# Optimization experiments

Measured on AMD Instinct MI355X. Metric: run time of the kernel, lower is better.

## Reference

```python
import jax, jax.numpy as jnp
import numpy as np

FP4_E2M1_VALUES = jnp.array([0.0, 0.5, 1.0, 1.5, 2.0, 3.0, 4.0, 6.0,
                             -0.0, -0.5, -1.0, -1.5, -2.0, -3.0, -4.0, -6.0],
                            dtype=jnp.float32)

OUT_F, IN_F, BS = 4096, 4096, 16


def setup_inputs() -> dict:
    key = jax.random.key(0)
    k1, k2, k3, k4 = jax.random.split(key, 4)
    x = jax.random.normal(k1, (4, 2048, IN_F), dtype=jnp.float32)
    weight_indices = jax.random.randint(k2, (OUT_F, IN_F // BS, BS), 0, 16, dtype=jnp.int32)
    weight_scales = jax.random.uniform(k3, (OUT_F, IN_F // BS), dtype=jnp.float32)
    bias = jax.random.normal(k4, (OUT_F,), dtype=jnp.float32)
    return {"x": x, "weight_indices": weight_indices,
            "weight_scales": weight_scales, "bias": bias}


def reference(x, weight_indices, weight_scales, bias):
    # Dequantize: gather FP4 values per index, scale per block of 16.
    idx = jnp.clip(weight_indices, 0, 15)              # [O, NB, BS]
    vals = FP4_E2M1_VALUES[idx]                        # [O, NB, BS]
    weight = (vals * weight_scales[:, :, None]).reshape(OUT_F, IN_F)
    # F.linear: y = x @ W^T + b
    return jnp.einsum('bsi,oi->bso', x, weight) + bias
```

## Files before the change

### kernel.cpp

```cpp
#include <hip/hip_runtime.h>
#include <hip/hip_bf16.h>

static constexpr int M_TOT = 8192;
static constexpr int N_TOT = 4096;
static constexpr int K_TOT = 4096;

static constexpr int BM = 256, BN = 256, BK = 32;
static constexpr int NT = K_TOT / BK;
static constexpr int GTHREADS = 512;
static constexpr int BUF_BYTES = 32768;
static constexpr int LDS_BYTES = 4 * BUF_BYTES;

typedef __bf16 bf16x8 __attribute__((ext_vector_type(8)));
typedef float f32x4 __attribute__((ext_vector_type(4)));
typedef unsigned short u16x8 __attribute__((ext_vector_type(8)));

__device__ __forceinline__ unsigned short f2bf(float f) {
  return __builtin_bit_cast(unsigned short, (__bf16)f);
}

__device__ __forceinline__ float fp4_decode(int idx) {
  unsigned u = (unsigned)idx & 15u;
  unsigned sgn = (u >> 3) << 31;
  unsigned mag = u & 7u;
  unsigned e = mag >> 1, m = mag & 1u;
  unsigned bits = (e == 0u) ? (m ? 0x3F000000u : 0u)
                            : (((126u + e) << 23) | (m << 22));
  return __uint_as_float(bits | sgn);
}

__device__ __forceinline__ void glds16(const void* g, void* l) {
  __builtin_amdgcn_global_load_lds(
      (__attribute__((address_space(1))) void*)g,
      (__attribute__((address_space(3))) void*)l, 16, 0, 0);
}

__global__ __launch_bounds__(256) void dequant_w_kernel(
    const int* __restrict__ idx, const float* __restrict__ scales,
    unsigned short* __restrict__ W) {
  const int t = blockIdx.x * 256 + threadIdx.x;
  const int4 v = reinterpret_cast<const int4*>(idx)[t];
  const float s = scales[t >> 2];
  ushort4 o;
  o.x = f2bf(fp4_decode(v.x) * s);
  o.y = f2bf(fp4_decode(v.y) * s);
  o.z = f2bf(fp4_decode(v.z) * s);
  o.w = f2bf(fp4_decode(v.w) * s);
  reinterpret_cast<ushort4*>(W)[t] = o;
}

__global__ __launch_bounds__(256) void convert_x_kernel(
    const float* __restrict__ x, unsigned short* __restrict__ A) {
  const int t = blockIdx.x * 256 + threadIdx.x;
  const float4* xp = reinterpret_cast<const float4*>(x);
  const float4 a = xp[2 * t], b = xp[2 * t + 1];
  u16x8 o;
  o[0] = f2bf(a.x); o[1] = f2bf(a.y); o[2] = f2bf(a.z); o[3] = f2bf(a.w);
  o[4] = f2bf(b.x); o[5] = f2bf(b.y); o[6] = f2bf(b.z); o[7] = f2bf(b.w);
  reinterpret_cast<u16x8*>(A)[t] = o;
}

__global__ __launch_bounds__(GTHREADS, 1) void gemm256(
    const unsigned short* __restrict__ A, const unsigned short* __restrict__ B,
    const float* __restrict__ bias, float* __restrict__ out) {
  extern __shared__ char smem[];

  const int t = threadIdx.x;
  const int lane = t & 63, wid = t >> 6;
  const int wr = wid >> 2;
  const int wc = wid & 3;
  const int ln = lane & 15;
  const int kc = lane >> 4;

  const int bid = blockIdx.x;
  const int bmi = (bid & 7) * 4 + ((bid >> 3) & 3);
  const int bni = bid >> 5;
  const int bm0 = bmi * BM, bn0 = bni * BN;

  const int row_s = t >> 2;
  const int kcd = (t & 3) ^ ((t >> 3) & 3);
  const unsigned short* gA = A + (size_t)(bm0 + row_s) * K_TOT + kcd * 8;
  const unsigned short* gB = B + (size_t)(bn0 + row_s) * K_TOT + kcd * 8;
  char* ldsA = smem + t * 16;
  char* ldsB = smem + 16384 + t * 16;

  const int swz = (kc ^ ((ln >> 1) & 3)) * 16;
  const int base_a = (wr * 128 + ln) * 64 + swz;
  const int base_b = 16384 + (wc * 64 + ln) * 64 + swz;

  f32x4 acc[8][4];
#pragma unroll
  for (int i = 0; i < 8; ++i)
#pragma unroll
    for (int j = 0; j < 4; ++j) acc[i][j] = f32x4{0.f, 0.f, 0.f, 0.f};

#define STAGE_A(kt, bufi) do {                                        \
    const unsigned short* s_ = gA + (size_t)(kt) * BK;                \
    glds16(s_, ldsA + (bufi) * BUF_BYTES);                            \
    glds16(s_ + (size_t)128 * K_TOT, ldsA + (bufi) * BUF_BYTES + 8192); \
  } while (0)
#define STAGE_B(kt, bufi) do {                                        \
    const unsigned short* s_ = gB + (size_t)(kt) * BK;                \
    glds16(s_, ldsB + (bufi) * BUF_BYTES);                            \
    glds16(s_ + (size_t)128 * K_TOT, ldsB + (bufi) * BUF_BYTES + 8192); \
  } while (0)

  bf16x8 af[4], bf[4];

#define LOAD_A4(bufi, mb) do {                                        \
    const char* pa_ = smem + (bufi) * BUF_BYTES + base_a + (mb) * 1024; \
    af[0] = *(const bf16x8*)(pa_);                                    \
    af[1] = *(const bf16x8*)(pa_ + 1024);                             \
    af[2] = *(const bf16x8*)(pa_ + 2048);                             \
    af[3] = *(const bf16x8*)(pa_ + 3072);                             \
  } while (0)
#define LOAD_B4(bufi) do {                                            \
    const char* pb_ = smem + (bufi) * BUF_BYTES + base_b;             \
    bf[0] = *(const bf16x8*)(pb_);                                    \
    bf[1] = *(const bf16x8*)(pb_ + 1024);                             \
    bf[2] = *(const bf16x8*)(pb_ + 2048);                             \
    bf[3] = *(const bf16x8*)(pb_ + 3072);                             \
  } while (0)

#define MFMA16(mb) do {                                               \
    __builtin_amdgcn_s_setprio(1);                                    \
    _Pragma("unroll")                                                 \
    for (int m_ = 0; m_ < 4; ++m_)                                    \
      _Pragma("unroll")                                               \
      for (int n_ = 0; n_ < 4; ++n_)                                  \
        acc[(mb) + m_][n_] = __builtin_amdgcn_mfma_f32_16x16x32_bf16( \
            af[m_], bf[n_], acc[(mb) + m_][n_], 0, 0, 0);             \
    __builtin_amdgcn_s_setprio(0);                                    \
  } while (0)

  STAGE_A(0, 0); STAGE_B(0, 0);
  asm volatile("" ::: "memory");
  STAGE_A(1, 1); STAGE_B(1, 1);
  asm volatile("" ::: "memory");
  STAGE_A(2, 2); STAGE_B(2, 2);
  asm volatile("s_waitcnt vmcnt(8)" ::: "memory");
  __builtin_amdgcn_s_barrier();

  for (int tt = 0; tt < NT - 3; ++tt) {
    const int cb = tt & 3, sb = (tt + 3) & 3;
    LOAD_A4(cb, 0);
    LOAD_B4(cb);
    STAGE_A(tt + 3, sb);
    __builtin_amdgcn_s_barrier();
    MFMA16(0);
    __builtin_amdgcn_s_barrier();
    LOAD_A4(cb, 4);
    STAGE_B(tt + 3, sb);
    __builtin_amdgcn_s_barrier();
    MFMA16(4);
    asm volatile("s_waitcnt vmcnt(8)" ::: "memory");
    __builtin_amdgcn_s_barrier();
  }

  for (int tt = NT - 3; tt < NT; ++tt) {
    const int cb = tt & 3;
    LOAD_A4(cb, 0);
    LOAD_B4(cb);
    __builtin_amdgcn_s_barrier();
    MFMA16(0);
    __builtin_amdgcn_s_barrier();
    LOAD_A4(cb, 4);
    __builtin_amdgcn_s_barrier();
    MFMA16(4);
    if (tt == NT - 3) asm volatile("s_waitcnt vmcnt(4)" ::: "memory");
    else if (tt == NT - 2) asm volatile("s_waitcnt vmcnt(0)" ::: "memory");
    __builtin_amdgcn_s_barrier();
  }

  const int orow0 = bm0 + wr * 128 + (lane >> 4) * 4;
  const int ocol0 = bn0 + wc * 64 + ln;
  float bj[4];
#pragma unroll
  for (int n = 0; n < 4; ++n) bj[n] = bias[ocol0 + n * 16];
#pragma unroll
  for (int mi = 0; mi < 8; ++mi)
#pragma unroll
    for (int n = 0; n < 4; ++n)
#pragma unroll
      for (int q = 0; q < 4; ++q)
        out[(size_t)(orow0 + mi * 16 + q) * N_TOT + ocol0 + n * 16] =
            acc[mi][n][q] + bj[n];
}

extern "C" void kernel_launch(void* const* d_in, const int* in_sizes, int n_in,
                              void* d_out, int out_size, void* d_ws, size_t ws_size,
                              hipStream_t stream) {
  const float* x = (const float*)d_in[0];
  const int* widx = (const int*)d_in[1];
  const float* wsc = (const float*)d_in[2];
  const float* bias = (const float*)d_in[3];
  float* out = (float*)d_out;

  unsigned short* Abf = (unsigned short*)d_ws;
  unsigned short* Wbf = (unsigned short*)((char*)d_ws + (size_t)M_TOT * K_TOT * 2);

  convert_x_kernel<<<dim3((M_TOT * (size_t)K_TOT / 8) / 256), dim3(256), 0, stream>>>(x, Abf);
  dequant_w_kernel<<<dim3((N_TOT * (size_t)K_TOT / 4) / 256), dim3(256), 0, stream>>>(widx, wsc, Wbf);

  (void)hipFuncSetAttribute((const void*)gemm256,
                            hipFuncAttributeMaxDynamicSharedMemorySize, LDS_BYTES);
  gemm256<<<dim3((M_TOT / BM) * (N_TOT / BN)), dim3(GTHREADS), LDS_BYTES, stream>>>(
      Abf, Wbf, bias, out);
}
```

Measured before the change: 292.7 us.

## Software-pipeline LDS fragment reads with double-buffered registers in GEMM main loop

```diff
diff --git a/kernel.cpp b/kernel.cpp
--- a/kernel.cpp
+++ b/kernel.cpp
@@ -94,43 +94,60 @@
 #pragma unroll
     for (int j = 0; j < 4; ++j) acc[i][j] = f32x4{0.f, 0.f, 0.f, 0.f};
 
-#define STAGE_A(kt, bufi) do {                                        \
-    const unsigned short* s_ = gA + (size_t)(kt) * BK;                \
-    glds16(s_, ldsA + (bufi) * BUF_BYTES);                            \
+  bf16x8 afA[4], afB[4], bfE[4], bfO[4];
+
+#define STAGE_A(kt, bufi) do {                                          \
+    const unsigned short* s_ = gA + (size_t)(kt) * BK;                  \
+    glds16(s_, ldsA + (bufi) * BUF_BYTES);                              \
     glds16(s_ + (size_t)128 * K_TOT, ldsA + (bufi) * BUF_BYTES + 8192); \
   } while (0)
-#define STAGE_B(kt, bufi) do {                                        \
-    const unsigned short* s_ = gB + (size_t)(kt) * BK;                \
-    glds16(s_, ldsB + (bufi) * BUF_BYTES);                            \
+#define STAGE_B(kt, bufi) do {                                          \
+    const unsigned short* s_ = gB + (size_t)(kt) * BK;                  \
+    glds16(s_, ldsB + (bufi) * BUF_BYTES);                              \
     glds16(s_ + (size_t)128 * K_TOT, ldsB + (bufi) * BUF_BYTES + 8192); \
   } while (0)
 
-  bf16x8 af[4], bf[4];
-
-#define LOAD_A4(bufi, mb) do {                                        \
-    const char* pa_ = smem + (bufi) * BUF_BYTES + base_a + (mb) * 1024; \
-    af[0] = *(const bf16x8*)(pa_);                                    \
-    af[1] = *(const bf16x8*)(pa_ + 1024);                             \
-    af[2] = *(const bf16x8*)(pa_ + 2048);                             \
-    af[3] = *(const bf16x8*)(pa_ + 3072);                             \
-  } while (0)
-#define LOAD_B4(bufi) do {                                            \
-    const char* pb_ = smem + (bufi) * BUF_BYTES + base_b;             \
-    bf[0] = *(const bf16x8*)(pb_);                                    \
-    bf[1] = *(const bf16x8*)(pb_ + 1024);                             \
-    bf[2] = *(const bf16x8*)(pb_ + 2048);                             \
-    bf[3] = *(const bf16x8*)(pb_ + 3072);                             \
-  } while (0)
-
-#define MFMA16(mb) do {                                               \
-    __builtin_amdgcn_s_setprio(1);                                    \
-    _Pragma("unroll")                                                 \
-    for (int m_ = 0; m_ < 4; ++m_)                                    \
-      _Pragma("unroll")                                               \
-      for (int n_ = 0; n_ < 4; ++n_)                                  \
-        acc[(mb) + m_][n_] = __builtin_amdgcn_mfma_f32_16x16x32_bf16( \
-            af[m_], bf[n_], acc[(mb) + m_][n_], 0, 0, 0);             \
-    __builtin_amdgcn_s_setprio(0);                                    \
+#define READ_AF(dst, bufi, mb) do {                                     \
+    const char* p_ = smem + (bufi) * BUF_BYTES + base_a + (mb) * 1024;  \
+    dst[0] = *(const bf16x8*)(p_);                                      \
+    dst[1] = *(const bf16x8*)(p_ + 1024);                               \
+    dst[2] = *(const bf16x8*)(p_ + 2048);                               \
+    dst[3] = *(const bf16x8*)(p_ + 3072);                               \
+  } while (0)
+#define READ_BF(dst, bufi) do {                                         \
+    const char* p_ = smem + (bufi) * BUF_BYTES + base_b;                \
+    dst[0] = *(const bf16x8*)(p_);                                      \
+    dst[1] = *(const bf16x8*)(p_ + 1024);                               \
+    dst[2] = *(const bf16x8*)(p_ + 2048);                               \
+    dst[3] = *(const bf16x8*)(p_ + 3072);                               \
+  } while (0)
+
+#define MFMA16(afs, bfs, mb) do {                                       \
+    __builtin_amdgcn_s_setprio(1);                                      \
+    _Pragma("unroll")                                                   \
+    for (int m_ = 0; m_ < 4; ++m_)                                      \
+      _Pragma("unroll")                                                 \
+      for (int n_ = 0; n_ < 4; ++n_)                                    \
+        acc[(mb) + m_][n_] = __builtin_amdgcn_mfma_f32_16x16x32_bf16(   \
+            afs[m_], bfs[n_], acc[(mb) + m_][n_], 0, 0, 0);             \
+    __builtin_amdgcn_s_setprio(0);                                      \
+  } while (0)
+
+#define VM(n) asm volatile("s_waitcnt vmcnt(" #n ")" ::: "memory")
+#define BAR __builtin_amdgcn_s_barrier()
+
+#define PH_A(tt, rb, sb, bfc) do { \
+    READ_AF(afB, rb, 4);           \
+    STAGE_A((tt) + 3, sb);         \
+    MFMA16(afA, bfc, 0);           \
+    VM(6); BAR;                    \
+  } while (0)
+#define PH_B(tt, rbn, sb, bfc, bfn) do { \
+    READ_AF(afA, rbn, 0);                \
+    READ_BF(bfn, rbn);                   \
+    STAGE_B((tt) + 3, sb);               \
+    MFMA16(afB, bfc, 4);                 \
+    BAR;                                 \
   } while (0)
 
   STAGE_A(0, 0); STAGE_B(0, 0);
@@ -138,39 +155,31 @@
   STAGE_A(1, 1); STAGE_B(1, 1);
   asm volatile("" ::: "memory");
   STAGE_A(2, 2); STAGE_B(2, 2);
-  asm volatile("s_waitcnt vmcnt(8)" ::: "memory");
-  __builtin_amdgcn_s_barrier();
-
-  for (int tt = 0; tt < NT - 3; ++tt) {
-    const int cb = tt & 3, sb = (tt + 3) & 3;
-    LOAD_A4(cb, 0);
-    LOAD_B4(cb);
-    STAGE_A(tt + 3, sb);
-    __builtin_amdgcn_s_barrier();
-    MFMA16(0);
-    __builtin_amdgcn_s_barrier();
-    LOAD_A4(cb, 4);
-    STAGE_B(tt + 3, sb);
-    __builtin_amdgcn_s_barrier();
-    MFMA16(4);
-    asm volatile("s_waitcnt vmcnt(8)" ::: "memory");
-    __builtin_amdgcn_s_barrier();
+  VM(8);
+  BAR;
+  READ_AF(afA, 0, 0);
+  READ_BF(bfE, 0);
+
+#pragma unroll 1
+  for (int tt = 0; tt < NT - 4; tt += 4) {
+    PH_A(tt + 0, 0, 3, bfE);
+    PH_B(tt + 0, 1, 3, bfE, bfO);
+    PH_A(tt + 1, 1, 0, bfO);
+    PH_B(tt + 1, 2, 0, bfO, bfE);
+    PH_A(tt + 2, 2, 1, bfE);
+    PH_B(tt + 2, 3, 1, bfE, bfO);
+    PH_A(tt + 3, 3, 2, bfO);
+    PH_B(tt + 3, 0, 2, bfO, bfE);
   }
 
-  for (int tt = NT - 3; tt < NT; ++tt) {
-    const int cb = tt & 3;
-    LOAD_A4(cb, 0);
-    LOAD_B4(cb);
-    __builtin_amdgcn_s_barrier();
-    MFMA16(0);
-    __builtin_amdgcn_s_barrier();
-    LOAD_A4(cb, 4);
-    __builtin_amdgcn_s_barrier();
-    MFMA16(4);
-    if (tt == NT - 3) asm volatile("s_waitcnt vmcnt(4)" ::: "memory");
-    else if (tt == NT - 2) asm volatile("s_waitcnt vmcnt(0)" ::: "memory");
-    __builtin_amdgcn_s_barrier();
-  }
+  READ_AF(afB, 0, 4); STAGE_A(127, 3); MFMA16(afA, bfE, 0); VM(6); BAR;
+  READ_AF(afA, 1, 0); READ_BF(bfO, 1); STAGE_B(127, 3); MFMA16(afB, bfE, 4); BAR;
+  READ_AF(afB, 1, 4); MFMA16(afA, bfO, 0); VM(4); BAR;
+  READ_AF(afA, 2, 0); READ_BF(bfE, 2); MFMA16(afB, bfO, 4); BAR;
+  READ_AF(afB, 2, 4); MFMA16(afA, bfE, 0); VM(0); BAR;
+  READ_AF(afA, 3, 0); READ_BF(bfO, 3); MFMA16(afB, bfE, 4); BAR;
+  READ_AF(afB, 3, 4); MFMA16(afA, bfO, 0);
+  MFMA16(afB, bfO, 4);
 
   const int orow0 = bm0 + wr * 128 + (lane >> 4) * 4;
   const int ocol0 = bn0 + wc * 64 + ln;
```

Measured after the change: 279.2 us. 4.6% less time.

## Shrink GEMM tile to 128x256 with 3-stage pipeline and higher occupancy

Applied to the files above, without the earlier changes.

```diff
diff --git a/kernel.cpp b/kernel.cpp
--- a/kernel.cpp
+++ b/kernel.cpp
@@ -5,11 +5,11 @@
 static constexpr int N_TOT = 4096;
 static constexpr int K_TOT = 4096;
 
-static constexpr int BM = 256, BN = 256, BK = 32;
+static constexpr int BM = 128, BN = 256, BK = 32;
 static constexpr int NT = K_TOT / BK;
 static constexpr int GTHREADS = 512;
-static constexpr int BUF_BYTES = 32768;
-static constexpr int LDS_BYTES = 4 * BUF_BYTES;
+static constexpr int BUF_BYTES = 24576;
+static constexpr int LDS_BYTES = 3 * BUF_BYTES;
 
 typedef __bf16 bf16x8 __attribute__((ext_vector_type(8)));
 typedef float f32x4 __attribute__((ext_vector_type(4)));
@@ -60,125 +60,110 @@
   reinterpret_cast<u16x8*>(A)[t] = o;
 }
 
-__global__ __launch_bounds__(GTHREADS, 1) void gemm256(
+__global__ __launch_bounds__(GTHREADS, 4) void gemm128x256(
     const unsigned short* __restrict__ A, const unsigned short* __restrict__ B,
     const float* __restrict__ bias, float* __restrict__ out) {
   extern __shared__ char smem[];
 
   const int t = threadIdx.x;
   const int lane = t & 63, wid = t >> 6;
-  const int wr = wid >> 2;
-  const int wc = wid & 3;
-  const int ln = lane & 15;
+  const int wrm = wid >> 2;
+  const int wcn = wid & 3;
+  const int l15 = lane & 15;
   const int kc = lane >> 4;
 
   const int bid = blockIdx.x;
-  const int bmi = (bid & 7) * 4 + ((bid >> 3) & 3);
-  const int bni = bid >> 5;
+  const int bmi = (bid & 7) * 8 + ((bid >> 3) & 7);
+  const int bni = bid >> 6;
   const int bm0 = bmi * BM, bn0 = bni * BN;
 
   const int row_s = t >> 2;
   const int kcd = (t & 3) ^ ((t >> 3) & 3);
   const unsigned short* gA = A + (size_t)(bm0 + row_s) * K_TOT + kcd * 8;
   const unsigned short* gB = B + (size_t)(bn0 + row_s) * K_TOT + kcd * 8;
-  char* ldsA = smem + t * 16;
-  char* ldsB = smem + 16384 + t * 16;
+  const unsigned short* gB1 = gB + (size_t)128 * K_TOT;
+  const int tid16 = t * 16;
 
-  const int swz = (kc ^ ((ln >> 1) & 3)) * 16;
-  const int base_a = (wr * 128 + ln) * 64 + swz;
-  const int base_b = 16384 + (wc * 64 + ln) * 64 + swz;
+  const int swz = (kc ^ ((l15 >> 1) & 3)) * 16;
+  const int base_a = (wrm * 64 + l15) * 64 + swz;
+  const int base_b = 8192 + (wcn * 64 + l15) * 64 + swz;
 
-  f32x4 acc[8][4];
+  f32x4 acc[4][4];
 #pragma unroll
-  for (int i = 0; i < 8; ++i)
+  for (int i = 0; i < 4; ++i)
 #pragma unroll
     for (int j = 0; j < 4; ++j) acc[i][j] = f32x4{0.f, 0.f, 0.f, 0.f};
 
-#define STAGE_A(kt, bufi) do {                                        \
-    const unsigned short* s_ = gA + (size_t)(kt) * BK;                \
-    glds16(s_, ldsA + (bufi) * BUF_BYTES);                            \
-    glds16(s_ + (size_t)128 * K_TOT, ldsA + (bufi) * BUF_BYTES + 8192); \
-  } while (0)
-#define STAGE_B(kt, bufi) do {                                        \
-    const unsigned short* s_ = gB + (size_t)(kt) * BK;                \
-    glds16(s_, ldsB + (bufi) * BUF_BYTES);                            \
-    glds16(s_ + (size_t)128 * K_TOT, ldsB + (bufi) * BUF_BYTES + 8192); \
+  bf16x8 af[4], bf[4];
+
+#define STG(kt, soff) do {                                   \
+    const int ko_ = (kt) * BK;                               \
+    glds16(gA + ko_, smem + (soff) + tid16);                 \
+    glds16(gB + ko_, smem + (soff) + 8192 + tid16);          \
+    glds16(gB1 + ko_, smem + (soff) + 16384 + tid16);        \
   } while (0)
 
-  bf16x8 af[4], bf[4];
-
-#define LOAD_A4(bufi, mb) do {                                        \
-    const char* pa_ = smem + (bufi) * BUF_BYTES + base_a + (mb) * 1024; \
-    af[0] = *(const bf16x8*)(pa_);                                    \
-    af[1] = *(const bf16x8*)(pa_ + 1024);                             \
-    af[2] = *(const bf16x8*)(pa_ + 2048);                             \
-    af[3] = *(const bf16x8*)(pa_ + 3072);                             \
-  } while (0)
-#define LOAD_B4(bufi) do {                                            \
-    const char* pb_ = smem + (bufi) * BUF_BYTES + base_b;             \
-    bf[0] = *(const bf16x8*)(pb_);                                    \
-    bf[1] = *(const bf16x8*)(pb_ + 1024);                             \
-    bf[2] = *(const bf16x8*)(pb_ + 2048);                             \
-    bf[3] = *(const bf16x8*)(pb_ + 3072);                             \
+#define RD(cboff) do {                                       \
+    const char* pa_ = smem + (cboff) + base_a;               \
+    const char* pb_ = smem + (cboff) + base_b;               \
+    af[0] = *(const bf16x8*)(pa_);                           \
+    af[1] = *(const bf16x8*)(pa_ + 1024);                    \
+    af[2] = *(const bf16x8*)(pa_ + 2048);                    \
+    af[3] = *(const bf16x8*)(pa_ + 3072);                    \
+    bf[0] = *(const bf16x8*)(pb_);                           \
+    bf[1] = *(const bf16x8*)(pb_ + 1024);                    \
+    bf[2] = *(const bf16x8*)(pb_ + 2048);                    \
+    bf[3] = *(const bf16x8*)(pb_ + 3072);                    \
   } while (0)
 
-#define MFMA16(mb) do {                                               \
-    __builtin_amdgcn_s_setprio(1);                                    \
-    _Pragma("unroll")                                                 \
-    for (int m_ = 0; m_ < 4; ++m_)                                    \
-      _Pragma("unroll")                                               \
-      for (int n_ = 0; n_ < 4; ++n_)                                  \
-        acc[(mb) + m_][n_] = __builtin_amdgcn_mfma_f32_16x16x32_bf16( \
-            af[m_], bf[n_], acc[(mb) + m_][n_], 0, 0, 0);             \
-    __builtin_amdgcn_s_setprio(0);                                    \
+#define MF16() do {                                          \
+    __builtin_amdgcn_s_setprio(1);                           \
+    _Pragma("unroll")                                        \
+    for (int m_ = 0; m_ < 4; ++m_)                           \
+      _Pragma("unroll")                                      \
+      for (int n_ = 0; n_ < 4; ++n_)                         \
+        acc[m_][n_] = __builtin_amdgcn_mfma_f32_16x16x32_bf16( \
+            af[m_], bf[n_], acc[m_][n_], 0, 0, 0);           \
+    __builtin_amdgcn_s_setprio(0);                           \
   } while (0)
 
-  STAGE_A(0, 0); STAGE_B(0, 0);
+#define VM(n) asm volatile("s_waitcnt vmcnt(" #n ")" ::: "memory")
+#define BAR __builtin_amdgcn_s_barrier()
+
+#define PH(tt, cboff, sboff) do {  \
+    RD(cboff);                     \
+    STG((tt) + 2, sboff);          \
+    MF16();                        \
+    VM(3); BAR;                    \
+  } while (0)
+
+  STG(0, 0);
   asm volatile("" ::: "memory");
-  STAGE_A(1, 1); STAGE_B(1, 1);
-  asm volatile("" ::: "memory");
-  STAGE_A(2, 2); STAGE_B(2, 2);
-  asm volatile("s_waitcnt vmcnt(8)" ::: "memory");
-  __builtin_amdgcn_s_barrier();
+  STG(1, BUF_BYTES);
+  VM(3);
+  BAR;
 
-  for (int tt = 0; tt < NT - 3; ++tt) {
-    const int cb = tt & 3, sb = (tt + 3) & 3;
-    LOAD_A4(cb, 0);
-    LOAD_B4(cb);
-    STAGE_A(tt + 3, sb);
-    __builtin_amdgcn_s_barrier();
-    MFMA16(0);
-    __builtin_amdgcn_s_barrier();
-    LOAD_A4(cb, 4);
-    STAGE_B(tt + 3, sb);
-    __builtin_amdgcn_s_barrier();
-    MFMA16(4);
-    asm volatile("s_waitcnt vmcnt(8)" ::: "memory");
-    __builtin_amdgcn_s_barrier();
+#pragma unroll 1
+  for (int i = 0; i < 42; ++i) {
+    const int T = 3 * i;
+    PH(T + 0, 0, 2 * BUF_BYTES);
+    PH(T + 1, BUF_BYTES, 0);
+    PH(T + 2, 2 * BUF_BYTES, BUF_BYTES);
   }
 
-  for (int tt = NT - 3; tt < NT; ++tt) {
-    const int cb = tt & 3;
-    LOAD_A4(cb, 0);
-    LOAD_B4(cb);
-    __builtin_amdgcn_s_barrier();
-    MFMA16(0);
-    __builtin_amdgcn_s_barrier();
-    LOAD_A4(cb, 4);
-    __builtin_amdgcn_s_barrier();
-    MFMA16(4);
-    if (tt == NT - 3) asm volatile("s_waitcnt vmcnt(4)" ::: "memory");
-    else if (tt == NT - 2) asm volatile("s_waitcnt vmcnt(0)" ::: "memory");
-    __builtin_amdgcn_s_barrier();
-  }
+  RD(0);
+  MF16();
+  VM(0); BAR;
+  RD(BUF_BYTES);
+  MF16();
 
-  const int orow0 = bm0 + wr * 128 + (lane >> 4) * 4;
-  const int ocol0 = bn0 + wc * 64 + ln;
+  const int orow0 = bm0 + wrm * 64 + (lane >> 4) * 4;
+  const int ocol0 = bn0 + wcn * 64 + l15;
   float bj[4];
 #pragma unroll
   for (int n = 0; n < 4; ++n) bj[n] = bias[ocol0 + n * 16];
 #pragma unroll
-  for (int mi = 0; mi < 8; ++mi)
+  for (int mi = 0; mi < 4; ++mi)
 #pragma unroll
     for (int n = 0; n < 4; ++n)
 #pragma unroll
@@ -202,8 +187,8 @@
   convert_x_kernel<<<dim3((M_TOT * (size_t)K_TOT / 8) / 256), dim3(256), 0, stream>>>(x, Abf);
   dequant_w_kernel<<<dim3((N_TOT * (size_t)K_TOT / 4) / 256), dim3(256), 0, stream>>>(widx, wsc, Wbf);
 
-  (void)hipFuncSetAttribute((const void*)gemm256,
+  (void)hipFuncSetAttribute((const void*)gemm128x256,
                             hipFuncAttributeMaxDynamicSharedMemorySize, LDS_BYTES);
-  gemm256<<<dim3((M_TOT / BM) * (N_TOT / BN)), dim3(GTHREADS), LDS_BYTES, stream>>>(
+  gemm128x256<<<dim3((M_TOT / BM) * (N_TOT / BN)), dim3(GTHREADS), LDS_BYTES, stream>>>(
       Abf, Wbf, bias, out);
 }
```

Result: slower. 314.7 us (+7.5%).
